# Performance work log

Measured on AMD Instinct MI355X. Metric: run time of the kernel, lower is better.

Reference implementation:

```python
import jax, jax.numpy as jnp
import numpy as np

NEG_FILL = -1.0e9
PROB_MIN = 1e-9


def _lstm_cell(x, h, c, w_ih, w_hh, b_ih, b_hh):
    # PyTorch gate order: input, forget, cell(g), output
    gates = x @ w_ih.T + h @ w_hh.T + b_ih + b_hh
    i, f, g, o = jnp.split(gates, 4, axis=-1)
    c_new = jax.nn.sigmoid(f) * c + jax.nn.sigmoid(i) * jnp.tanh(g)
    h_new = jax.nn.sigmoid(o) * jnp.tanh(c_new)
    return h_new, c_new


def setup_inputs() -> dict:
    key = jax.random.key(0)
    B, T, D, H, W = 2048, 100, 128, 256, 256
    ks = jax.random.split(key, 16)
    s_d = 1.0 / np.sqrt(D)
    s_h = 1.0 / np.sqrt(H)
    s_w = 1.0 / np.sqrt(W)
    return {
        "targets": jax.random.normal(ks[0], (B, T, D), jnp.float32),
        "h0": jax.random.normal(ks[1], (1, B, H), jnp.float32),
        "c0": jax.random.normal(ks[2], (1, B, H), jnp.float32),
        "enc_w_ih": jax.random.normal(ks[3], (4 * H, D), jnp.float32) * s_d,
        "enc_w_hh": jax.random.normal(ks[4], (4 * H, H), jnp.float32) * s_h,
        "enc_b_ih": jax.random.normal(ks[5], (4 * H,), jnp.float32) * s_h,
        "enc_b_hh": jax.random.normal(ks[6], (4 * H,), jnp.float32) * s_h,
        "dec_w_ih": jax.random.normal(ks[7], (4 * H, D), jnp.float32) * s_d,
        "dec_w_hh": jax.random.normal(ks[8], (4 * H, H), jnp.float32) * s_h,
        "dec_b_ih": jax.random.normal(ks[9], (4 * H,), jnp.float32) * s_h,
        "dec_b_hh": jax.random.normal(ks[10], (4 * H,), jnp.float32) * s_h,
        "W1": jax.random.normal(ks[11], (W, H), jnp.float32) * s_h,
        "W2": jax.random.normal(ks[12], (W, H), jnp.float32) * s_h,
        "vt": jax.random.normal(ks[13], (W,), jnp.float32) * s_w,
    }


def reference(targets, h0, c0, enc_w_ih, enc_w_hh, enc_b_ih, enc_b_hh,
              dec_w_ih, dec_w_hh, dec_b_ih, dec_b_hh, W1, W2, vt):
    B, T, D = targets.shape
    H = enc_w_hh.shape[1]

    # ---- encoder LSTM (batch_first, zero initial state) ----
    def enc_step(carry, x_t):
        h, c = carry
        h, c = _lstm_cell(x_t, h, c, enc_w_ih, enc_w_hh, enc_b_ih, enc_b_hh)
        return (h, c), h

    z = jnp.zeros((B, H), targets.dtype)
    _, enc_h = jax.lax.scan(enc_step, (z, z), jnp.swapaxes(targets, 0, 1))
    encoder_states = jnp.swapaxes(enc_h, 0, 1)  # [B, T, H]

    blend1 = encoder_states @ W1.T  # [B, T, W]

    a1 = jnp.arange(B)
    init = (h0[0], c0[0], jnp.zeros((B, T), dtype=bool), jnp.zeros_like(targets[:, 0]))

    def dec_step(carry, _):
        h, c, selected, dec_in = carry
        h, c = _lstm_cell(dec_in, h, c, dec_w_ih, dec_w_hh, dec_b_ih, dec_b_hh)
        blend2 = h @ W2.T                                   # [B, W]
        scores = jnp.tanh(blend1 + blend2[:, None, :]) @ vt  # [B, T]
        scores = jnp.where(selected, NEG_FILL, scores)
        sel = jnp.argmax(scores, axis=-1)                    # [B]
        selected = selected.at[a1, sel].set(True)
        probs = jnp.maximum(jax.nn.softmax(scores, axis=-1), PROB_MIN)
        dec_in = targets[a1, sel]                            # [B, D]
        return (h, c, selected, dec_in), probs

    _, probs = jax.lax.scan(dec_step, init, None, length=T)
    return jnp.swapaxes(probs, 0, 1)  # [B, T, T]
```

## Files before the change

### kernel.cpp

```cpp
#include <hip/hip_runtime.h>
#include <math.h>

#define BB   2048
#define TT   100
#define DD   128
#define HH   256
#define NEGF -1.0e9f

__device__ __forceinline__ float sigmoidf_(float x){ return 1.0f/(1.0f+expf(-x)); }

__device__ __forceinline__ float tanh_fast(float x){
  x = fminf(15.f, fmaxf(-15.f, x));
  const float e = __expf(x + x);
  return (e - 1.f) * __builtin_amdgcn_rcpf(e + 1.f);
}

__global__ __launch_bounds__(256) void k_zero_i32(int* __restrict__ p, int n){
  int i = blockIdx.x*256 + threadIdx.x;
  if(i < n) p[i] = 0;
}

__global__ __launch_bounds__(128) void k_gates_cell(
    const float* __restrict__ Xp, int ldx,
    const float* __restrict__ Hp,
    const float* __restrict__ Wih, const float* __restrict__ Whh,
    const float* __restrict__ bih, const float* __restrict__ bhh,
    const float* __restrict__ Cp,
    float* __restrict__ Hout, float* __restrict__ Cout,
    float* __restrict__ Hcopy, int hstride)
{
  __shared__ alignas(16) float Xs[32*68];
  __shared__ alignas(16) float Ws[32*68];
  const int tid = threadIdx.x;
  const int tx = tid & 15;
  const int ty = tid >> 4;
  const int j0 = blockIdx.x * 16;
  const int m0 = blockIdx.y * 64;

  float acc[8][4];
  #pragma unroll
  for(int i=0;i<8;i++)
    #pragma unroll
    for(int s=0;s<4;s++) acc[i][s] = 0.f;

  for(int phase=0; phase<2; phase++){
    const float* Am; int lda; const float* Wm; int ldw; int nt;
    if(phase==0){ if(!Xp) continue; Am=Xp; lda=ldx; Wm=Wih; ldw=DD; nt=4; }
    else        { if(!Hp) continue; Am=Hp; lda=HH;  Wm=Whh; ldw=HH; nt=8; }
    for(int kt=0; kt<nt; kt++){
      const int k0 = kt*32;
      #pragma unroll
      for(int it=0; it<4; it++){
        int q = it*128 + tid; int m = q>>3; int kq = (q&7)<<2;
        const float4 v = *(const float4*)(Am + (size_t)(m0+m)*lda + k0 + kq);
        Xs[(kq+0)*68+m]=v.x; Xs[(kq+1)*68+m]=v.y; Xs[(kq+2)*68+m]=v.z; Xs[(kq+3)*68+m]=v.w;
      }
      #pragma unroll
      for(int it=0; it<4; it++){
        int q = it*128 + tid; int c = q>>3; int kq = (q&7)<<2;
        int n = (c&3)*HH + j0 + (c>>2);
        const float4 v = *(const float4*)(Wm + (size_t)n*ldw + k0 + kq);
        Ws[(kq+0)*68+c]=v.x; Ws[(kq+1)*68+c]=v.y; Ws[(kq+2)*68+c]=v.z; Ws[(kq+3)*68+c]=v.w;
      }
      __syncthreads();
      #pragma unroll
      for(int kk=0; kk<32; kk++){
        const float4 a0 = *(const float4*)&Xs[kk*68 + ty*8];
        const float4 a1 = *(const float4*)&Xs[kk*68 + ty*8 + 4];
        const float4 bv = *(const float4*)&Ws[kk*68 + tx*4];
        const float a[8] = {a0.x,a0.y,a0.z,a0.w,a1.x,a1.y,a1.z,a1.w};
        const float g[4] = {bv.x,bv.y,bv.z,bv.w};
        #pragma unroll
        for(int i=0;i<8;i++)
          #pragma unroll
          for(int s=0;s<4;s++)
            acc[i][s] = fmaf(a[i], g[s], acc[i][s]);
      }
      __syncthreads();
    }
  }

  const int col = j0 + tx;
  const float bi0 = bih[       col] + bhh[       col];
  const float bf0 = bih[  HH + col] + bhh[  HH + col];
  const float bg0 = bih[2*HH + col] + bhh[2*HH + col];
  const float bo0 = bih[3*HH + col] + bhh[3*HH + col];
  #pragma unroll
  for(int i=0;i<8;i++){
    const int b = m0 + ty*8 + i;
    const size_t idx = (size_t)b*HH + col;
    const float iv = acc[i][0] + bi0;
    const float fv = acc[i][1] + bf0;
    const float gv = acc[i][2] + bg0;
    const float ov = acc[i][3] + bo0;
    const float cp = Cp ? Cp[idx] : 0.f;
    const float cn = sigmoidf_(fv)*cp + sigmoidf_(iv)*tanhf(gv);
    const float hn = sigmoidf_(ov)*tanhf(cn);
    Cout[idx] = cn;
    Hout[idx] = hn;
    if(Hcopy) Hcopy[(size_t)b*hstride + col] = hn;
  }
}

__global__ __launch_bounds__(256) void k_gemm_nt(
    const float* __restrict__ A, int lda,
    const float* __restrict__ Bm, int ldb,
    float* __restrict__ C, int ldc, int K)
{
  __shared__ alignas(16) float Xs[32*68];
  __shared__ alignas(16) float Ws[32*68];
  const int tid = threadIdx.x;
  const int tx = tid & 15, ty = tid >> 4;
  const int n0 = blockIdx.x*64, m0 = blockIdx.y*64;
  float acc[4][4];
  #pragma unroll
  for(int i=0;i<4;i++)
    #pragma unroll
    for(int j=0;j<4;j++) acc[i][j]=0.f;

  for(int k0=0; k0<K; k0+=32){
    #pragma unroll
    for(int it=0; it<2; it++){
      int q = it*256 + tid; int m = q>>3; int kq = (q&7)<<2;
      float4 v = *(const float4*)(A + (size_t)(m0+m)*lda + k0 + kq);
      Xs[(kq+0)*68+m]=v.x; Xs[(kq+1)*68+m]=v.y; Xs[(kq+2)*68+m]=v.z; Xs[(kq+3)*68+m]=v.w;
      v = *(const float4*)(Bm + (size_t)(n0+m)*ldb + k0 + kq);
      Ws[(kq+0)*68+m]=v.x; Ws[(kq+1)*68+m]=v.y; Ws[(kq+2)*68+m]=v.z; Ws[(kq+3)*68+m]=v.w;
    }
    __syncthreads();
    #pragma unroll
    for(int kk=0; kk<32; kk++){
      const float4 av = *(const float4*)&Xs[kk*68 + ty*4];
      const float4 bv = *(const float4*)&Ws[kk*68 + tx*4];
      const float a[4] = {av.x,av.y,av.z,av.w};
      const float b[4] = {bv.x,bv.y,bv.z,bv.w};
      #pragma unroll
      for(int i=0;i<4;i++)
        #pragma unroll
        for(int j=0;j<4;j++)
          acc[i][j] = fmaf(a[i], b[j], acc[i][j]);
    }
    __syncthreads();
  }
  #pragma unroll
  for(int i=0;i<4;i++){
    *(float4*)&C[(size_t)(m0+ty*4+i)*ldc + n0 + tx*4] =
        make_float4(acc[i][0],acc[i][1],acc[i][2],acc[i][3]);
  }
}

__global__ __launch_bounds__(256) void k_blend1(float* __restrict__ blend1,
                                                const float* __restrict__ W1)
{
  __shared__ alignas(16) float Af[32*260];
  __shared__ alignas(16) float Ws[32*68];
  const int tid = threadIdx.x;
  const int tx = tid & 15, ty = tid >> 4;
  const size_t r0 = (size_t)blockIdx.x * 32;

  #pragma unroll
  for(int it=0; it<8; it++){
    int q = it*256 + tid; int m = q>>6; int kq = (q&63)<<2;
    *(float4*)&Af[m*260 + kq] = *(const float4*)(blend1 + (r0+m)*256 + kq);
  }
  __syncthreads();

  for(int nc=0; nc<4; nc++){
    const int n0 = nc*64;
    float acc[2][4];
    #pragma unroll
    for(int i=0;i<2;i++)
      #pragma unroll
      for(int j=0;j<4;j++) acc[i][j]=0.f;
    for(int kt=0; kt<8; kt++){
      const int k0 = kt*32;
      __syncthreads();
      #pragma unroll
      for(int it=0; it<2; it++){
        int q = it*256 + tid; int c = q>>3; int kq = (q&7)<<2;
        const float4 v = *(const float4*)(W1 + (size_t)(n0+c)*256 + k0 + kq);
        Ws[(kq+0)*68+c]=v.x; Ws[(kq+1)*68+c]=v.y; Ws[(kq+2)*68+c]=v.z; Ws[(kq+3)*68+c]=v.w;
      }
      __syncthreads();
      #pragma unroll
      for(int kk=0; kk<32; kk++){
        const float4 bv = *(const float4*)&Ws[kk*68 + tx*4];
        const float a0 = Af[(ty*2+0)*260 + k0 + kk];
        const float a1 = Af[(ty*2+1)*260 + k0 + kk];
        acc[0][0]=fmaf(a0,bv.x,acc[0][0]); acc[0][1]=fmaf(a0,bv.y,acc[0][1]);
        acc[0][2]=fmaf(a0,bv.z,acc[0][2]); acc[0][3]=fmaf(a0,bv.w,acc[0][3]);
        acc[1][0]=fmaf(a1,bv.x,acc[1][0]); acc[1][1]=fmaf(a1,bv.y,acc[1][1]);
        acc[1][2]=fmaf(a1,bv.z,acc[1][2]); acc[1][3]=fmaf(a1,bv.w,acc[1][3]);
      }
    }
    #pragma unroll
    for(int i=0;i<2;i++){
      *(float4*)&blend1[(r0 + ty*2 + i)*256 + n0 + tx*4] =
          make_float4(acc[i][0],acc[i][1],acc[i][2],acc[i][3]);
    }
  }
}

__global__ __launch_bounds__(256) void k_scores(
    const float* __restrict__ blend1,
    const float* __restrict__ blend2,
    const float* __restrict__ vt,
    const float* __restrict__ targets,
    int*  __restrict__ selected,
    float* __restrict__ dec_in,
    float* __restrict__ out,
    int s)
{
  __shared__ float vt_s[256], b2_s[256], sc[128];
  __shared__ float M_s, S_s;
  __shared__ int sel_s;
  const int b = blockIdx.x;
  const int tid = threadIdx.x;
  const int lane = tid & 63;
  const int wave = tid >> 6;

  vt_s[tid] = vt[tid];
  b2_s[tid] = blend2[(size_t)b*256 + tid];
  __syncthreads();

  const float4 bb = *(const float4*)&b2_s[lane*4];
  const float4 vv = *(const float4*)&vt_s[lane*4];

  for(int it=0; it<25; it++){
    const int t = wave + it*4;
    const float4 x = *(const float4*)(blend1 + ((size_t)b*TT + t)*256 + lane*4);
    float p;
    p = tanh_fast(x.x + bb.x) * vv.x;
    p = fmaf(tanh_fast(x.y + bb.y), vv.y, p);
    p = fmaf(tanh_fast(x.z + bb.z), vv.z, p);
    p = fmaf(tanh_fast(x.w + bb.w), vv.w, p);
    #pragma unroll
    for(int off=32; off>=1; off>>=1) p += __shfl_xor(p, off, 64);
    if(lane == 0) sc[t] = p;
  }
  __syncthreads();

  if(wave == 0){
    float m1 = selected[(size_t)b*TT + lane] ? NEGF : sc[lane];
    sc[lane] = m1;
    float bestv = m1; int besti = lane;
    float m2 = 0.f;
    const int t2 = lane + 64;
    if(t2 < TT){
      m2 = selected[(size_t)b*TT + t2] ? NEGF : sc[t2];
      sc[t2] = m2;
      if(m2 > bestv){ bestv = m2; besti = t2; }
    }
    #pragma unroll
    for(int off=32; off>=1; off>>=1){
      const float ov = __shfl_xor(bestv, off, 64);
      const int   oi = __shfl_xor(besti, off, 64);
      if(ov > bestv || (ov == bestv && oi < besti)){ bestv = ov; besti = oi; }
    }
    float e = __expf(m1 - bestv);
    if(t2 < TT) e += __expf(m2 - bestv);
    #pragma unroll
    for(int off=32; off>=1; off>>=1) e += __shfl_xor(e, off, 64);
    if(lane == 0){
      M_s = bestv; S_s = e; sel_s = besti;
      selected[(size_t)b*TT + besti] = 1;
    }
  }
  __syncthreads();

  const int sel = sel_s;
  if(tid < TT){
    float p = __expf(sc[tid] - M_s) / S_s;
    out[(size_t)b*TT*TT + (size_t)s*TT + tid] = fmaxf(p, 1e-9f);
  }
  if(tid < DD){
    dec_in[(size_t)b*DD + tid] = targets[((size_t)b*TT + sel)*DD + tid];
  }
}

extern "C" void kernel_launch(void* const* d_in, const int* in_sizes, int n_in,
                              void* d_out, int out_size, void* d_ws, size_t ws_size,
                              hipStream_t stream)
{
  (void)in_sizes; (void)n_in; (void)out_size; (void)ws_size;
  const float* targets  = (const float*)d_in[0];
  const float* h0       = (const float*)d_in[1];
  const float* c0       = (const float*)d_in[2];
  const float* enc_w_ih = (const float*)d_in[3];
  const float* enc_w_hh = (const float*)d_in[4];
  const float* enc_b_ih = (const float*)d_in[5];
  const float* enc_b_hh = (const float*)d_in[6];
  const float* dec_w_ih = (const float*)d_in[7];
  const float* dec_w_hh = (const float*)d_in[8];
  const float* dec_b_ih = (const float*)d_in[9];
  const float* dec_b_hh = (const float*)d_in[10];
  const float* W1       = (const float*)d_in[11];
  const float* W2       = (const float*)d_in[12];
  const float* vt       = (const float*)d_in[13];
  float* out = (float*)d_out;

  float* ws      = (float*)d_ws;
  float* blend1  = ws;
  float* hA      = blend1 + (size_t)BB*TT*256;
  float* hB      = hA + (size_t)BB*HH;
  float* cA      = hB + (size_t)BB*HH;
  float* cB      = cA + (size_t)BB*HH;
  float* blend2  = cB + (size_t)BB*HH;
  float* dec_in  = blend2 + (size_t)BB*HH;
  int*   selected= (int*)(dec_in + (size_t)BB*DD);

  k_zero_i32<<<(BB*TT + 255)/256, 256, 0, stream>>>(selected, BB*TT);

  for(int t=0; t<TT; t++){
    const float* Hp = (t==0) ? nullptr : ((t&1) ? hA : hB);
    const float* Cp = (t==0) ? nullptr : ((t&1) ? cA : cB);
    float* Ho = (t&1) ? hB : hA;
    float* Co = (t&1) ? cB : cA;
    k_gates_cell<<<dim3(16,32), 128, 0, stream>>>(
        targets + (size_t)t*DD, TT*DD,
        Hp, enc_w_ih, enc_w_hh, enc_b_ih, enc_b_hh, Cp,
        Ho, Co, blend1 + (size_t)t*256, TT*256);
  }

  k_blend1<<<BB*TT/32, 256, 0, stream>>>(blend1, W1);

  for(int s=0; s<TT; s++){
    const float* Hp = (s==0) ? h0 : ((s&1) ? hA : hB);
    const float* Cp = (s==0) ? c0 : ((s&1) ? cA : cB);
    float* Ho = (s&1) ? hB : hA;
    float* Co = (s&1) ? cB : cA;
    const float* Xp = (s==0) ? nullptr : dec_in;
    k_gates_cell<<<dim3(16,32), 128, 0, stream>>>(
        Xp, DD, Hp, dec_w_ih, dec_w_hh, dec_b_ih, dec_b_hh, Cp,
        Ho, Co, nullptr, 0);
    k_gemm_nt<<<dim3(4,32), 256, 0, stream>>>(Ho, HH, W2, HH, blend2, HH, HH);
    k_scores<<<BB, 256, 0, stream>>>(blend1, blend2, vt, targets, selected,
                                     dec_in, out, s);
  }
}
```

Before: 14.24 ms.

## Move LSTM and blend GEMMs onto bf16 MFMA with three-way split precision

Replaces the FP32 FMA GEMMs in the LSTM gate cell, the blend1 projection and the blend2 projection with bf16 MFMA 16x16x32 instructions. Each FP32 operand is split into three bf16 parts (hi/mid/lo), and six cross products are accumulated to keep roughly FP32 accuracy. Weights are pre-split once per call into a workspace; activations are split on the fly when loaded into shared memory. This trades six MFMAs per tile plus split arithmetic and extra LDS traffic for much higher matrix throughput, at some risk to numerics near argmax ties.

```diff
diff --git a/kernel.cpp b/kernel.cpp
--- a/kernel.cpp
+++ b/kernel.cpp
@@ -1,5 +1,6 @@
 #include <hip/hip_runtime.h>
 #include <math.h>
+#include <stdint.h>
 
 #define BB   2048
 #define TT   100
@@ -7,6 +8,11 @@
 #define HH   256
 #define NEGF -1.0e9f
 
+typedef __attribute__((ext_vector_type(8))) short short8_t;
+typedef __attribute__((ext_vector_type(4))) float f32x4;
+
+#define MFMA16(a,b,c) __builtin_amdgcn_mfma_f32_16x16x32_bf16((a),(b),(c),0,0,0)
+
 __device__ __forceinline__ float sigmoidf_(float x){ return 1.0f/(1.0f+expf(-x)); }
 
 __device__ __forceinline__ float tanh_fast(float x){
@@ -15,190 +21,280 @@
   return (e - 1.f) * __builtin_amdgcn_rcpf(e + 1.f);
 }
 
+__device__ __forceinline__ void bf16_split3(float x, unsigned short &h,
+                                            unsigned short &m, unsigned short &l){
+  const unsigned u = __float_as_uint(x);
+  const unsigned r = u + 0x7FFFu + ((u >> 16) & 1u);
+  h = (unsigned short)(r >> 16);
+  const float rem = x - __uint_as_float(r & 0xFFFF0000u);
+  const unsigned u2 = __float_as_uint(rem);
+  const unsigned r2 = u2 + 0x7FFFu + ((u2 >> 16) & 1u);
+  m = (unsigned short)(r2 >> 16);
+  const float rem2 = rem - __uint_as_float(r2 & 0xFFFF0000u);
+  l = (unsigned short)(__float_as_uint(rem2) >> 16);
+}
+
+__global__ __launch_bounds__(256) void k_split3(const float* __restrict__ src,
+    unsigned short* __restrict__ hi, unsigned short* __restrict__ mi,
+    unsigned short* __restrict__ lo, int n){
+  const int i = blockIdx.x*256 + threadIdx.x;
+  if(i < n){ unsigned short h,m,l; bf16_split3(src[i], h, m, l);
+             hi[i]=h; mi[i]=m; lo[i]=l; }
+}
+
 __global__ __launch_bounds__(256) void k_zero_i32(int* __restrict__ p, int n){
   int i = blockIdx.x*256 + threadIdx.x;
   if(i < n) p[i] = 0;
 }
 
+#define MFMA_X6(aH,aM,aL,bH,bM,bL,acc)            \
+  do{ acc = MFMA16(aM, bM, acc);                  \
+      acc = MFMA16(aH, bL, acc);                  \
+      acc = MFMA16(aL, bH, acc);                  \
+      acc = MFMA16(aH, bM, acc);                  \
+      acc = MFMA16(aM, bH, acc);                  \
+      acc = MFMA16(aH, bH, acc); }while(0)
+
 __global__ __launch_bounds__(128) void k_gates_cell(
     const float* __restrict__ Xp, int ldx,
     const float* __restrict__ Hp,
-    const float* __restrict__ Wih, const float* __restrict__ Whh,
+    const unsigned short* __restrict__ WihH, const unsigned short* __restrict__ WihM,
+    const unsigned short* __restrict__ WihL,
+    const unsigned short* __restrict__ WhhH, const unsigned short* __restrict__ WhhM,
+    const unsigned short* __restrict__ WhhL,
     const float* __restrict__ bih, const float* __restrict__ bhh,
     const float* __restrict__ Cp,
     float* __restrict__ Hout, float* __restrict__ Cout,
     float* __restrict__ Hcopy, int hstride)
 {
-  __shared__ alignas(16) float Xs[32*68];
-  __shared__ alignas(16) float Ws[32*68];
-  const int tid = threadIdx.x;
-  const int tx = tid & 15;
-  const int ty = tid >> 4;
-  const int j0 = blockIdx.x * 16;
-  const int m0 = blockIdx.y * 64;
-
-  float acc[8][4];
-  #pragma unroll
-  for(int i=0;i<8;i++)
-    #pragma unroll
-    for(int s=0;s<4;s++) acc[i][s] = 0.f;
+  __shared__ alignas(16) unsigned short AsH[64*40], AsM[64*40], AsL[64*40];
+  __shared__ alignas(16) unsigned short WsH[64*40], WsM[64*40], WsL[64*40];
+  const int tid  = threadIdx.x;
+  const int lane = tid & 63;
+  const int wv   = tid >> 6;
+  const int l15  = lane & 15;
+  const int l4   = lane >> 4;
+  const int j0   = blockIdx.x * 16;
+  const int m0   = blockIdx.y * 64;
+
+  f32x4 acc[2][4];
+  #pragma unroll
+  for(int a=0;a<2;a++)
+    #pragma unroll
+    for(int s=0;s<4;s++)
+      #pragma unroll
+      for(int e=0;e<4;e++) acc[a][s][e] = 0.f;
 
   for(int phase=0; phase<2; phase++){
-    const float* Am; int lda; const float* Wm; int ldw; int nt;
-    if(phase==0){ if(!Xp) continue; Am=Xp; lda=ldx; Wm=Wih; ldw=DD; nt=4; }
-    else        { if(!Hp) continue; Am=Hp; lda=HH;  Wm=Whh; ldw=HH; nt=8; }
+    const float* Am; int lda;
+    const unsigned short *WH, *WM, *WL; int ldw, nt;
+    if(phase==0){ if(!Xp) continue; Am=Xp; lda=ldx;
+                  WH=WihH; WM=WihM; WL=WihL; ldw=DD; nt=4; }
+    else        { if(!Hp) continue; Am=Hp; lda=HH;
+                  WH=WhhH; WM=WhhM; WL=WhhL; ldw=HH; nt=8; }
     for(int kt=0; kt<nt; kt++){
       const int k0 = kt*32;
+      __syncthreads();
       #pragma unroll
       for(int it=0; it<4; it++){
-        int q = it*128 + tid; int m = q>>3; int kq = (q&7)<<2;
-        const float4 v = *(const float4*)(Am + (size_t)(m0+m)*lda + k0 + kq);
-        Xs[(kq+0)*68+m]=v.x; Xs[(kq+1)*68+m]=v.y; Xs[(kq+2)*68+m]=v.z; Xs[(kq+3)*68+m]=v.w;
+        const int q  = it*128 + tid;
+        const int r  = q >> 3;
+        const int kq = (q & 7) << 2;
+        const float4 v = *(const float4*)(Am + (size_t)(m0+r)*lda + k0 + kq);
+        unsigned short h0,m0_,l0,h1,m1_,l1,h2,m2_,l2,h3,m3_,l3;
+        bf16_split3(v.x,h0,m0_,l0); bf16_split3(v.y,h1,m1_,l1);
+        bf16_split3(v.z,h2,m2_,l2); bf16_split3(v.w,h3,m3_,l3);
+        *(ushort4*)&AsH[r*40+kq] = make_ushort4(h0,h1,h2,h3);
+        *(ushort4*)&AsM[r*40+kq] = make_ushort4(m0_,m1_,m2_,m3_);
+        *(ushort4*)&AsL[r*40+kq] = make_ushort4(l0,l1,l2,l3);
       }
       #pragma unroll
-      for(int it=0; it<4; it++){
-        int q = it*128 + tid; int c = q>>3; int kq = (q&7)<<2;
-        int n = (c&3)*HH + j0 + (c>>2);
-        const float4 v = *(const float4*)(Wm + (size_t)n*ldw + k0 + kq);
-        Ws[(kq+0)*68+c]=v.x; Ws[(kq+1)*68+c]=v.y; Ws[(kq+2)*68+c]=v.z; Ws[(kq+3)*68+c]=v.w;
+      for(int half=0; half<3; half++){
+        const unsigned short* __restrict__ Wg = (half==0)?WH:((half==1)?WM:WL);
+        unsigned short* Ws = (half==0)?WsH:((half==1)?WsM:WsL);
+        #pragma unroll
+        for(int it=0; it<2; it++){
+          const int q  = it*128 + tid;
+          const int c  = q >> 2;
+          const int kq = (q & 3) << 3;
+          const int n  = ((c>>4)*HH) + j0 + (c & 15);
+          *(uint4*)&Ws[c*40+kq] = *(const uint4*)(Wg + (size_t)n*ldw + k0 + kq);
+        }
       }
       __syncthreads();
-      #pragma unroll
-      for(int kk=0; kk<32; kk++){
-        const float4 a0 = *(const float4*)&Xs[kk*68 + ty*8];
-        const float4 a1 = *(const float4*)&Xs[kk*68 + ty*8 + 4];
-        const float4 bv = *(const float4*)&Ws[kk*68 + tx*4];
-        const float a[8] = {a0.x,a0.y,a0.z,a0.w,a1.x,a1.y,a1.z,a1.w};
-        const float g[4] = {bv.x,bv.y,bv.z,bv.w};
+      short8_t aH[2], aM[2], aL[2];
+      #pragma unroll
+      for(int fm=0; fm<2; fm++){
+        const int r = wv*32 + fm*16 + l15;
+        aH[fm] = *(const short8_t*)&AsH[r*40 + l4*8];
+        aM[fm] = *(const short8_t*)&AsM[r*40 + l4*8];
+        aL[fm] = *(const short8_t*)&AsL[r*40 + l4*8];
+      }
+      #pragma unroll
+      for(int s=0; s<4; s++){
+        const int c = s*16 + l15;
+        const short8_t bH = *(const short8_t*)&WsH[c*40 + l4*8];
+        const short8_t bM = *(const short8_t*)&WsM[c*40 + l4*8];
+        const short8_t bL = *(const short8_t*)&WsL[c*40 + l4*8];
         #pragma unroll
-        for(int i=0;i<8;i++)
-          #pragma unroll
-          for(int s=0;s<4;s++)
-            acc[i][s] = fmaf(a[i], g[s], acc[i][s]);
+        for(int fm=0; fm<2; fm++){
+          MFMA_X6(aH[fm],aM[fm],aL[fm], bH,bM,bL, acc[fm][s]);
+        }
       }
-      __syncthreads();
-    }
-  }
-
-  const int col = j0 + tx;
-  const float bi0 = bih[       col] + bhh[       col];
-  const float bf0 = bih[  HH + col] + bhh[  HH + col];
-  const float bg0 = bih[2*HH + col] + bhh[2*HH + col];
-  const float bo0 = bih[3*HH + col] + bhh[3*HH + col];
-  #pragma unroll
-  for(int i=0;i<8;i++){
-    const int b = m0 + ty*8 + i;
-    const size_t idx = (size_t)b*HH + col;
-    const float iv = acc[i][0] + bi0;
-    const float fv = acc[i][1] + bf0;
-    const float gv = acc[i][2] + bg0;
-    const float ov = acc[i][3] + bo0;
-    const float cp = Cp ? Cp[idx] : 0.f;
-    const float cn = sigmoidf_(fv)*cp + sigmoidf_(iv)*tanhf(gv);
-    const float hn = sigmoidf_(ov)*tanhf(cn);
-    Cout[idx] = cn;
-    Hout[idx] = hn;
-    if(Hcopy) Hcopy[(size_t)b*hstride + col] = hn;
-  }
-}
-
-__global__ __launch_bounds__(256) void k_gemm_nt(
-    const float* __restrict__ A, int lda,
-    const float* __restrict__ Bm, int ldb,
-    float* __restrict__ C, int ldc, int K)
+    }
+  }
+
+  const int j = j0 + l15;
+  const float bi0 = bih[       j] + bhh[       j];
+  const float bf0 = bih[  HH + j] + bhh[  HH + j];
+  const float bg0 = bih[2*HH + j] + bhh[2*HH + j];
+  const float bo0 = bih[3*HH + j] + bhh[3*HH + j];
+  #pragma unroll
+  for(int fm=0; fm<2; fm++){
+    #pragma unroll
+    for(int r=0; r<4; r++){
+      const int m = m0 + wv*32 + fm*16 + l4*4 + r;
+      const size_t idx = (size_t)m*HH + j;
+      const float iv = acc[fm][0][r] + bi0;
+      const float fv = acc[fm][1][r] + bf0;
+      const float gv = acc[fm][2][r] + bg0;
+      const float ov = acc[fm][3][r] + bo0;
+      const float cp = Cp ? Cp[idx] : 0.f;
+      const float cn = sigmoidf_(fv)*cp + sigmoidf_(iv)*tanhf(gv);
+      const float hn = sigmoidf_(ov)*tanhf(cn);
+      Cout[idx] = cn;
+      Hout[idx] = hn;
+      if(Hcopy) Hcopy[(size_t)m*hstride + j] = hn;
+    }
+  }
+}
+
+__global__ __launch_bounds__(128) void k_blend2(
+    const float* __restrict__ Hin,
+    const unsigned short* __restrict__ W2H, const unsigned short* __restrict__ W2M,
+    const unsigned short* __restrict__ W2L,
+    float* __restrict__ out)
 {
-  __shared__ alignas(16) float Xs[32*68];
-  __shared__ alignas(16) float Ws[32*68];
-  const int tid = threadIdx.x;
-  const int tx = tid & 15, ty = tid >> 4;
-  const int n0 = blockIdx.x*64, m0 = blockIdx.y*64;
-  float acc[4][4];
-  #pragma unroll
-  for(int i=0;i<4;i++)
-    #pragma unroll
-    for(int j=0;j<4;j++) acc[i][j]=0.f;
-
-  for(int k0=0; k0<K; k0+=32){
+  __shared__ alignas(16) unsigned short AsH[32*40], AsM[32*40], AsL[32*40];
+  __shared__ alignas(16) unsigned short WsH[64*40], WsM[64*40], WsL[64*40];
+  const int tid  = threadIdx.x;
+  const int lane = tid & 63;
+  const int wv   = tid >> 6;
+  const int l15  = lane & 15;
+  const int l4   = lane >> 4;
+  const int n0   = blockIdx.x * 64;
+  const int m0   = blockIdx.y * 32;
+
+  f32x4 acc[4];
+  #pragma unroll
+  for(int s=0;s<4;s++)
+    #pragma unroll
+    for(int e=0;e<4;e++) acc[s][e] = 0.f;
+
+  for(int kt=0; kt<8; kt++){
+    const int k0 = kt*32;
+    __syncthreads();
     #pragma unroll
     for(int it=0; it<2; it++){
-      int q = it*256 + tid; int m = q>>3; int kq = (q&7)<<2;
-      float4 v = *(const float4*)(A + (size_t)(m0+m)*lda + k0 + kq);
-      Xs[(kq+0)*68+m]=v.x; Xs[(kq+1)*68+m]=v.y; Xs[(kq+2)*68+m]=v.z; Xs[(kq+3)*68+m]=v.w;
-      v = *(const float4*)(Bm + (size_t)(n0+m)*ldb + k0 + kq);
-      Ws[(kq+0)*68+m]=v.x; Ws[(kq+1)*68+m]=v.y; Ws[(kq+2)*68+m]=v.z; Ws[(kq+3)*68+m]=v.w;
+      const int q  = it*128 + tid;
+      const int r  = q >> 3;
+      const int kq = (q & 7) << 2;
+      const float4 v = *(const float4*)(Hin + (size_t)(m0+r)*HH + k0 + kq);
+      unsigned short h0,m0_,l0,h1,m1_,l1,h2,m2_,l2,h3,m3_,l3;
+      bf16_split3(v.x,h0,m0_,l0); bf16_split3(v.y,h1,m1_,l1);
+      bf16_split3(v.z,h2,m2_,l2); bf16_split3(v.w,h3,m3_,l3);
+      *(ushort4*)&AsH[r*40+kq] = make_ushort4(h0,h1,h2,h3);
+      *(ushort4*)&AsM[r*40+kq] = make_ushort4(m0_,m1_,m2_,m3_);
+      *(ushort4*)&AsL[r*40+kq] = make_ushort4(l0,l1,l2,l3);
+    }
+    #pragma unroll
+    for(int half=0; half<3; half++){
+      const unsigned short* __restrict__ Wg = (half==0)?W2H:((half==1)?W2M:W2L);
+      unsigned short* Ws = (half==0)?WsH:((half==1)?WsM:WsL);
+      #pragma unroll
+      for(int it=0; it<2; it++){
+        const int q  = it*128 + tid;
+        const int c  = q >> 2;
+        const int kq = (q & 3) << 3;
+        const int n  = n0 + c;
+        *(uint4*)&Ws[c*40+kq] = *(const uint4*)(Wg + (size_t)n*HH + k0 + kq);
+      }
     }
     __syncthreads();
-    #pragma unroll
-    for(int kk=0; kk<32; kk++){
-      const float4 av = *(const float4*)&Xs[kk*68 + ty*4];
-      const float4 bv = *(const float4*)&Ws[kk*68 + tx*4];
-      const float a[4] = {av.x,av.y,av.z,av.w};
-      const float b[4] = {bv.x,bv.y,bv.z,bv.w};
-      #pragma unroll
-      for(int i=0;i<4;i++)
-        #pragma unroll
-        for(int j=0;j<4;j++)
-          acc[i][j] = fmaf(a[i], b[j], acc[i][j]);
-    }
-    __syncthreads();
-  }
-  #pragma unroll
-  for(int i=0;i<4;i++){
-    *(float4*)&C[(size_t)(m0+ty*4+i)*ldc + n0 + tx*4] =
-        make_float4(acc[i][0],acc[i][1],acc[i][2],acc[i][3]);
-  }
-}
-
-__global__ __launch_bounds__(256) void k_blend1(float* __restrict__ blend1,
-                                                const float* __restrict__ W1)
+    const int r = wv*16 + l15;
+    const short8_t aH = *(const short8_t*)&AsH[r*40 + l4*8];
+    const short8_t aM = *(const short8_t*)&AsM[r*40 + l4*8];
+    const short8_t aL = *(const short8_t*)&AsL[r*40 + l4*8];
+    #pragma unroll
+    for(int s=0; s<4; s++){
+      const int c = s*16 + l15;
+      const short8_t bH = *(const short8_t*)&WsH[c*40 + l4*8];
+      const short8_t bM = *(const short8_t*)&WsM[c*40 + l4*8];
+      const short8_t bL = *(const short8_t*)&WsL[c*40 + l4*8];
+      MFMA_X6(aH,aM,aL, bH,bM,bL, acc[s]);
+    }
+  }
+  #pragma unroll
+  for(int s=0; s<4; s++)
+    #pragma unroll
+    for(int r=0; r<4; r++)
+      out[(size_t)(m0 + wv*16 + l4*4 + r)*HH + n0 + s*16 + l15] = acc[s][r];
+}
+
+__global__ __launch_bounds__(128) void k_blend1(
+    float* __restrict__ blend1,
+    const unsigned short* __restrict__ W1H, const unsigned short* __restrict__ W1M,
+    const unsigned short* __restrict__ W1L)
 {
-  __shared__ alignas(16) float Af[32*260];
-  __shared__ alignas(16) float Ws[32*68];
-  const int tid = threadIdx.x;
-  const int tx = tid & 15, ty = tid >> 4;
+  __shared__ alignas(16) unsigned short AsH[32*264], AsM[32*264], AsL[32*264];
+  const int tid  = threadIdx.x;
+  const int lane = tid & 63;
+  const int wv   = tid >> 6;
+  const int l15  = lane & 15;
+  const int l4   = lane >> 4;
   const size_t r0 = (size_t)blockIdx.x * 32;
 
   #pragma unroll
-  for(int it=0; it<8; it++){
-    int q = it*256 + tid; int m = q>>6; int kq = (q&63)<<2;
-    *(float4*)&Af[m*260 + kq] = *(const float4*)(blend1 + (r0+m)*256 + kq);
+  for(int it=0; it<16; it++){
+    const int q  = it*128 + tid;
+    const int r  = q >> 6;
+    const int kq = (q & 63) << 2;
+    const float4 v = *(const float4*)(blend1 + (r0+r)*256 + kq);
+    unsigned short h0,m0_,l0,h1,m1_,l1,h2,m2_,l2,h3,m3_,l3;
+    bf16_split3(v.x,h0,m0_,l0); bf16_split3(v.y,h1,m1_,l1);
+    bf16_split3(v.z,h2,m2_,l2); bf16_split3(v.w,h3,m3_,l3);
+    *(ushort4*)&AsH[r*264+kq] = make_ushort4(h0,h1,h2,h3);
+    *(ushort4*)&AsM[r*264+kq] = make_ushort4(m0_,m1_,m2_,m3_);
+    *(ushort4*)&AsL[r*264+kq] = make_ushort4(l0,l1,l2,l3);
   }
   __syncthreads();
 
-  for(int nc=0; nc<4; nc++){
-    const int n0 = nc*64;
-    float acc[2][4];
-    #pragma unroll
-    for(int i=0;i<2;i++)
-      #pragma unroll
-      for(int j=0;j<4;j++) acc[i][j]=0.f;
-    for(int kt=0; kt<8; kt++){
-      const int k0 = kt*32;
-      __syncthreads();
-      #pragma unroll
-      for(int it=0; it<2; it++){
-        int q = it*256 + tid; int c = q>>3; int kq = (q&7)<<2;
-        const float4 v = *(const float4*)(W1 + (size_t)(n0+c)*256 + k0 + kq);
-        Ws[(kq+0)*68+c]=v.x; Ws[(kq+1)*68+c]=v.y; Ws[(kq+2)*68+c]=v.z; Ws[(kq+3)*68+c]=v.w;
-      }
-      __syncthreads();
-      #pragma unroll
-      for(int kk=0; kk<32; kk++){
-        const float4 bv = *(const float4*)&Ws[kk*68 + tx*4];
-        const float a0 = Af[(ty*2+0)*260 + k0 + kk];
-        const float a1 = Af[(ty*2+1)*260 + k0 + kk];
-        acc[0][0]=fmaf(a0,bv.x,acc[0][0]); acc[0][1]=fmaf(a0,bv.y,acc[0][1]);
-        acc[0][2]=fmaf(a0,bv.z,acc[0][2]); acc[0][3]=fmaf(a0,bv.w,acc[0][3]);
-        acc[1][0]=fmaf(a1,bv.x,acc[1][0]); acc[1][1]=fmaf(a1,bv.y,acc[1][1]);
-        acc[1][2]=fmaf(a1,bv.z,acc[1][2]); acc[1][3]=fmaf(a1,bv.w,acc[1][3]);
-      }
-    }
-    #pragma unroll
-    for(int i=0;i<2;i++){
-      *(float4*)&blend1[(r0 + ty*2 + i)*256 + n0 + tx*4] =
-          make_float4(acc[i][0],acc[i][1],acc[i][2],acc[i][3]);
-    }
-  }
+  f32x4 acc[16];
+  #pragma unroll
+  for(int s=0;s<16;s++)
+    #pragma unroll
+    for(int e=0;e<4;e++) acc[s][e] = 0.f;
+
+  const int rb = wv*16;
+  for(int kt=0; kt<8; kt++){
+    const int k0 = kt*32;
+    const short8_t aH = *(const short8_t*)&AsH[(rb+l15)*264 + k0 + l4*8];
+    const short8_t aM = *(const short8_t*)&AsM[(rb+l15)*264 + k0 + l4*8];
+    const short8_t aL = *(const short8_t*)&AsL[(rb+l15)*264 + k0 + l4*8];
+    #pragma unroll
+    for(int fn=0; fn<16; fn++){
+      const int n = fn*16 + l15;
+      const short8_t bH = *(const short8_t*)(W1H + (size_t)n*256 + k0 + l4*8);
+      const short8_t bM = *(const short8_t*)(W1M + (size_t)n*256 + k0 + l4*8);
+      const short8_t bL = *(const short8_t*)(W1L + (size_t)n*256 + k0 + l4*8);
+      MFMA_X6(aH,aM,aL, bH,bM,bL, acc[fn]);
+    }
+  }
+  #pragma unroll
+  for(int fn=0; fn<16; fn++)
+    #pragma unroll
+    for(int r=0; r<4; r++)
+      blend1[(r0 + rb + l4*4 + r)*256 + fn*16 + l15] = acc[fn][r];
 }
 
 __global__ __launch_bounds__(256) void k_scores(
@@ -309,6 +405,35 @@
   float* dec_in  = blend2 + (size_t)BB*HH;
   int*   selected= (int*)(dec_in + (size_t)BB*DD);
 
+  char* pc = (char*)(selected + (size_t)BB*TT);
+  pc = (char*)(((uintptr_t)pc + 63) & ~(uintptr_t)63);
+  unsigned short* q = (unsigned short*)pc;
+  unsigned short* ewihH = q; q += (size_t)1024*128;
+  unsigned short* ewihM = q; q += (size_t)1024*128;
+  unsigned short* ewihL = q; q += (size_t)1024*128;
+  unsigned short* ewhhH = q; q += (size_t)1024*256;
+  unsigned short* ewhhM = q; q += (size_t)1024*256;
+  unsigned short* ewhhL = q; q += (size_t)1024*256;
+  unsigned short* dwihH = q; q += (size_t)1024*128;
+  unsigned short* dwihM = q; q += (size_t)1024*128;
+  unsigned short* dwihL = q; q += (size_t)1024*128;
+  unsigned short* dwhhH = q; q += (size_t)1024*256;
+  unsigned short* dwhhM = q; q += (size_t)1024*256;
+  unsigned short* dwhhL = q; q += (size_t)1024*256;
+  unsigned short* w1H   = q; q += (size_t)256*256;
+  unsigned short* w1M   = q; q += (size_t)256*256;
+  unsigned short* w1L   = q; q += (size_t)256*256;
+  unsigned short* w2H   = q; q += (size_t)256*256;
+  unsigned short* w2M   = q; q += (size_t)256*256;
+  unsigned short* w2L   = q; q += (size_t)256*256;
+
+  k_split3<<<(1024*128+255)/256, 256, 0, stream>>>(enc_w_ih, ewihH, ewihM, ewihL, 1024*128);
+  k_split3<<<(1024*256+255)/256, 256, 0, stream>>>(enc_w_hh, ewhhH, ewhhM, ewhhL, 1024*256);
+  k_split3<<<(1024*128+255)/256, 256, 0, stream>>>(dec_w_ih, dwihH, dwihM, dwihL, 1024*128);
+  k_split3<<<(1024*256+255)/256, 256, 0, stream>>>(dec_w_hh, dwhhH, dwhhM, dwhhL, 1024*256);
+  k_split3<<<(256*256+255)/256,  256, 0, stream>>>(W1, w1H, w1M, w1L, 256*256);
+  k_split3<<<(256*256+255)/256,  256, 0, stream>>>(W2, w2H, w2M, w2L, 256*256);
+
   k_zero_i32<<<(BB*TT + 255)/256, 256, 0, stream>>>(selected, BB*TT);
 
   for(int t=0; t<TT; t++){
@@ -318,11 +443,11 @@
     float* Co = (t&1) ? cB : cA;
     k_gates_cell<<<dim3(16,32), 128, 0, stream>>>(
         targets + (size_t)t*DD, TT*DD,
-        Hp, enc_w_ih, enc_w_hh, enc_b_ih, enc_b_hh, Cp,
+        Hp, ewihH, ewihM, ewihL, ewhhH, ewhhM, ewhhL, enc_b_ih, enc_b_hh, Cp,
         Ho, Co, blend1 + (size_t)t*256, TT*256);
   }
 
-  k_blend1<<<BB*TT/32, 256, 0, stream>>>(blend1, W1);
+  k_blend1<<<BB*TT/32, 128, 0, stream>>>(blend1, w1H, w1M, w1L);
 
   for(int s=0; s<TT; s++){
     const float* Hp = (s==0) ? h0 : ((s&1) ? hA : hB);
@@ -331,9 +456,9 @@
     float* Co = (s&1) ? cB : cA;
     const float* Xp = (s==0) ? nullptr : dec_in;
     k_gates_cell<<<dim3(16,32), 128, 0, stream>>>(
-        Xp, DD, Hp, dec_w_ih, dec_w_hh, dec_b_ih, dec_b_hh, Cp,
+        Xp, DD, Hp, dwihH, dwihM, dwihL, dwhhH, dwhhM, dwhhL, dec_b_ih, dec_b_hh, Cp,
         Ho, Co, nullptr, 0);
-    k_gemm_nt<<<dim3(4,32), 256, 0, stream>>>(Ho, HH, W2, HH, blend2, HH, HH);
+    k_blend2<<<dim3(4,64), 128, 0, stream>>>(Ho, w2H, w2M, w2L, blend2);
     k_scores<<<BB, 256, 0, stream>>>(blend1, blend2, vt, targets, selected,
                                      dec_in, out, s);
   }
```

After: 14.68 ms. 1.03x slower.
